# Kernel optimization log

Measured on AMD Instinct MI355X. Metric: run time of the kernel, lower is better.

## Reference

```python
import jax, jax.numpy as jnp
import numpy as np

N = 100000      # nodes
E = 1600000     # edges (avg degree 16)
D = 64          # in_dim == hidden_dim
L = 4           # layer_gin
G = 128         # graphs in batch
BN_EPS = 1e-5


def setup_inputs() -> dict:
    key = jax.random.key(0)
    ks = jax.random.split(key, 9)
    x = jax.random.normal(ks[0], (N, D), dtype=jnp.float32)
    edge_index = jax.random.randint(ks[1], (2, E), 0, N, dtype=jnp.int32)
    batch = jnp.sort(jax.random.randint(ks[2], (N,), 0, G, dtype=jnp.int32))
    s = 0.05
    W1 = jax.random.normal(ks[3], (L, D, D), dtype=jnp.float32) * s
    b1 = jax.random.normal(ks[4], (L, D), dtype=jnp.float32) * s
    gamma = jnp.ones((L, D), dtype=jnp.float32)
    beta = jnp.zeros((L, D), dtype=jnp.float32)
    W2 = jax.random.normal(ks[5], (L, D, D), dtype=jnp.float32) * s
    b2 = jax.random.normal(ks[6], (L, D), dtype=jnp.float32) * s
    return dict(x=x, edge_index=edge_index, batch=batch,
                W1=W1, b1=b1, gamma=gamma, beta=beta, W2=W2, b2=b2)


def reference(x, edge_index, batch, W1, b1, gamma, beta, W2, b2):
    n = x.shape[0]
    src, dst = edge_index[0], edge_index[1]  # flow source_to_target
    # in-degree for mean aggregation (clamped to avoid div-by-zero)
    deg = jax.ops.segment_sum(jnp.ones(src.shape, x.dtype), dst, num_segments=n)
    inv_deg = 1.0 / jnp.maximum(deg, 1.0)
    # graph sizes for global mean pool
    gcnt = jax.ops.segment_sum(jnp.ones((n,), x.dtype), batch, num_segments=G)
    inv_gcnt = 1.0 / jnp.maximum(gcnt, 1.0)

    h = x
    node_pool = jnp.zeros((n, W2.shape[-1]), x.dtype)
    g_pool = jnp.zeros((G, W2.shape[-1]), x.dtype)
    for l in range(L):  # small fixed layer count
        # scatter-mean neighbor aggregation: [E,D] gather -> segment_sum
        agg = jax.ops.segment_sum(h[src], dst, num_segments=n) * inv_deg[:, None]
        z = (h + agg) @ W1[l] + b1[l]          # eps=0: (1+eps)*x + mean_j x_j
        mu = z.mean(axis=0)
        var = z.var(axis=0)                     # biased, as torch BatchNorm1d
        z = (z - mu) * jax.lax.rsqrt(var + BN_EPS) * gamma[l] + beta[l]
        h = jax.nn.relu(z) @ W2[l] + b2[l]
        node_pool = node_pool + h
        g_pool = g_pool + jax.ops.segment_sum(h, batch, num_segments=G) * inv_gcnt[:, None]
    return node_pool, g_pool
```

## Files before the change

kernel.cpp:

```cpp
#include <hip/hip_runtime.h>

#define N_NODES 100000
#define N_EDGES 1600000
#define DIM 64
#define NLAYER 4
#define NGRAPH 128
#define BN_EPS 1e-5f
#define NSHARD 16

typedef unsigned short ushort_t;
typedef unsigned int uint_t;

__device__ __forceinline__ ushort_t f2bf(float f) {
    uint_t u = __float_as_uint(f);
    uint_t r = (u + 0x7FFFu + ((u >> 16) & 1u)) >> 16;
    return (ushort_t)r;
}

__device__ __forceinline__ void bf8_to_f32(const uint4 v, float f[8]) {
    f[0] = __uint_as_float(v.x << 16);
    f[1] = __uint_as_float(v.x & 0xFFFF0000u);
    f[2] = __uint_as_float(v.y << 16);
    f[3] = __uint_as_float(v.y & 0xFFFF0000u);
    f[4] = __uint_as_float(v.z << 16);
    f[5] = __uint_as_float(v.z & 0xFFFF0000u);
    f[6] = __uint_as_float(v.w << 16);
    f[7] = __uint_as_float(v.w & 0xFFFF0000u);
}


__global__ void k_hist(const int* __restrict__ ei, int* __restrict__ cntS,
                       int* __restrict__ rank) {
    int e = blockIdx.x * blockDim.x + threadIdx.x;
    if (e < N_EDGES) {
        int d = ei[N_EDGES + e];
        int s = blockIdx.x & (NSHARD - 1);
        rank[e] = atomicAdd(&cntS[s * N_NODES + d], 1);
    }
}

__global__ void k_sumsh(int* __restrict__ cntS, int* __restrict__ cnt) {
    int i = blockIdx.x * blockDim.x + threadIdx.x;
    if (i < N_NODES) {
        int run = 0;
#pragma unroll
        for (int s = 0; s < NSHARD; s++) {
            int c = cntS[s * N_NODES + i];
            cntS[s * N_NODES + i] = run;
            run += c;
        }
        cnt[i] = run;
    }
}

__global__ void k_scan1(const int* __restrict__ cnt, int* __restrict__ exc,
                        int* __restrict__ bsums) {
    __shared__ int s[256];
    int i = blockIdx.x * 256 + threadIdx.x;
    int v = (i < N_NODES) ? cnt[i] : 0;
    s[threadIdx.x] = v;
    __syncthreads();
    for (int off = 1; off < 256; off <<= 1) {
        int t = (threadIdx.x >= off) ? s[threadIdx.x - off] : 0;
        __syncthreads();
        s[threadIdx.x] += t;
        __syncthreads();
    }
    if (i < N_NODES) exc[i] = s[threadIdx.x] - v;
    if (threadIdx.x == 255) bsums[blockIdx.x] = s[255];
}

__global__ void k_scan2(const int* __restrict__ bsums, int* __restrict__ boffs, int nb) {
    __shared__ int s[512];
    int v = ((int)threadIdx.x < nb) ? bsums[threadIdx.x] : 0;
    s[threadIdx.x] = v;
    __syncthreads();
    for (int off = 1; off < 512; off <<= 1) {
        int t = (threadIdx.x >= off) ? s[threadIdx.x - off] : 0;
        __syncthreads();
        s[threadIdx.x] += t;
        __syncthreads();
    }
    if ((int)threadIdx.x < nb) boffs[threadIdx.x] = s[threadIdx.x] - v;
}

__global__ void k_scan3(int* __restrict__ exc, const int* __restrict__ boffs) {
    int i = blockIdx.x * 256 + threadIdx.x;
    if (i < N_NODES) exc[i] += boffs[blockIdx.x];
}

__global__ void k_fill(const int* __restrict__ ei, const int* __restrict__ rowptr,
                       const int* __restrict__ cntS, const int* __restrict__ rank,
                       int* __restrict__ csr) {
    int e = blockIdx.x * blockDim.x + threadIdx.x;
    if (e < N_EDGES) {
        int d = ei[N_EDGES + e];
        int s = blockIdx.x & (NSHARD - 1);
        csr[rowptr[d] + cntS[s * N_NODES + d] + rank[e]] = ei[e];
    }
}

__global__ void k_prep(const int* __restrict__ cnt, const int* __restrict__ batch,
                       float* __restrict__ invdeg, float* __restrict__ invg) {
    int i = blockIdx.x * blockDim.x + threadIdx.x;
    if (i < N_NODES) invdeg[i] = 1.0f / (float)max(cnt[i], 1);
    if (i < NGRAPH) {
        int key = i, lo = 0, hi = N_NODES;
        while (lo < hi) { int m = (lo + hi) >> 1; if (batch[m] < key) lo = m + 1; else hi = m; }
        int a = lo;
        key = i + 1; lo = 0; hi = N_NODES;
        while (lo < hi) { int m = (lo + hi) >> 1; if (batch[m] < key) lo = m + 1; else hi = m; }
        invg[i] = 1.0f / (float)max(lo - a, 1);
    }
}

__global__ void k_xcast(const float* __restrict__ x, ushort_t* __restrict__ xh) {
    int i = blockIdx.x * blockDim.x + threadIdx.x;
    if (i < N_NODES * 16) {
        const float4 v = ((const float4*)x)[i];
        ushort4 u;
        u.x = f2bf(v.x); u.y = f2bf(v.y); u.z = f2bf(v.z); u.w = f2bf(v.w);
        ((ushort4*)xh)[i] = u;
    }
}

__device__ __forceinline__ void grp8b(const ushort_t* __restrict__ h,
                                      const int* __restrict__ cp,
                                      int e, int deg, int q, int r,
                                      float acc[8]) {
    const int last = deg - 1;
    const int e0 = e + q;
    int i0 = cp[min(e0, last)];
    float m0 = (e0 < deg) ? 1.f : 0.f;
    const uint4 v = *(const uint4*)(h + (size_t)i0 * 64 + r * 8);
    float f[8];
    bf8_to_f32(v, f);
#pragma unroll
    for (int j = 0; j < 8; j++) acc[j] = fmaf(f[j], m0, acc[j]);
}


#define CHUNK_A 14

__global__ __launch_bounds__(256, 4)
void k_passA(const ushort_t* __restrict__ h, const float* __restrict__ W1,
             const float* __restrict__ b1,
             const int* __restrict__ rowptr, const int* __restrict__ cnt,
             const int* __restrict__ csr, const float* __restrict__ invdeg,
             float* __restrict__ z, float* __restrict__ colsum,
             float* __restrict__ colsumsq) {
    const int lane = threadIdx.x & 63;
    const int q = lane >> 3;
    const int r = lane & 7;
    int wid_raw = (blockIdx.x << 2) | (threadIdx.x >> 6);
    const int wid = __builtin_amdgcn_readfirstlane(wid_raw);
    const int n0 = wid * CHUNK_A;
    const int n1 = min(N_NODES, n0 + CHUNK_A);

    float w[64];
#pragma unroll
    for (int k = 0; k < 64; k++) w[k] = W1[k * 64 + lane];
#pragma unroll
    for (int k = 0; k < 64; k++) asm("" : "+v"(w[k]));
    const float bj = b1[lane];

    float ls = 0.f, lq = 0.f;
    for (int n = n0; n + 2 <= n1; n += 2) {
        const int sa = rowptr[n],     da = cnt[n];
        const int sb = rowptr[n + 1], db = cnt[n + 1];
        const float idga = invdeg[n], idgb = invdeg[n + 1];
        const int* __restrict__ ca = csr + sa;
        const int* __restrict__ cb = csr + sb;

        float aa[8] = {0,0,0,0,0,0,0,0};
        float ab[8] = {0,0,0,0,0,0,0,0};
        const int m = min(da, db);
        int e = 0;
        for (; e < m; e += 8) {
            grp8b(h, ca, e, da, q, r, aa);
            grp8b(h, cb, e, db, q, r, ab);
        }
        for (; e < da; e += 8) grp8b(h, ca, e, da, q, r, aa);
        for (; e < db; e += 8) grp8b(h, cb, e, db, q, r, ab);

#pragma unroll
        for (int j = 0; j < 8; j++) {
            aa[j] += __shfl_xor(aa[j], 8, 64);
            aa[j] += __shfl_xor(aa[j], 16, 64);
            aa[j] += __shfl_xor(aa[j], 32, 64);
            ab[j] += __shfl_xor(ab[j], 8, 64);
            ab[j] += __shfl_xor(ab[j], 16, 64);
            ab[j] += __shfl_xor(ab[j], 32, 64);
        }

        const uint4 sva = *(const uint4*)(h + (size_t)n * 64 + r * 8);
        const uint4 svb = *(const uint4*)(h + (size_t)(n + 1) * 64 + r * 8);
        float sa8[8], sb8[8];
        bf8_to_f32(sva, sa8);
        bf8_to_f32(svb, sb8);
        float ta[8], tb[8];
#pragma unroll
        for (int j = 0; j < 8; j++) {
            ta[j] = fmaf(aa[j], idga, sa8[j]);
            tb[j] = fmaf(ab[j], idgb, sb8[j]);
        }

        float za = bj, zb = bj;
#pragma unroll
        for (int rr = 0; rr < 8; rr++) {
#pragma unroll
            for (int j = 0; j < 8; j++) {
                float ka = __int_as_float(__builtin_amdgcn_readlane(__float_as_int(ta[j]), rr));
                float kb = __int_as_float(__builtin_amdgcn_readlane(__float_as_int(tb[j]), rr));
                za = fmaf(ka, w[rr * 8 + j], za);
                zb = fmaf(kb, w[rr * 8 + j], zb);
            }
        }
        z[(size_t)n * 64 + lane] = za;
        z[(size_t)(n + 1) * 64 + lane] = zb;
        ls += za + zb;
        lq += za * za + zb * zb;
    }

    __shared__ float rs[256], rq[256];
    rs[threadIdx.x] = ls;
    rq[threadIdx.x] = lq;
    __syncthreads();
    if (threadIdx.x < 64) {
        float a = rs[threadIdx.x] + rs[threadIdx.x + 64] + rs[threadIdx.x + 128] + rs[threadIdx.x + 192];
        float b = rq[threadIdx.x] + rq[threadIdx.x + 64] + rq[threadIdx.x + 128] + rq[threadIdx.x + 192];
        atomicAdd(&colsum[threadIdx.x], a);
        atomicAdd(&colsumsq[threadIdx.x], b);
    }
}


__global__ void k_bnprep(float* __restrict__ colsum, float* __restrict__ colsumsq,
                         const float* __restrict__ gamma, const float* __restrict__ beta,
                         float* __restrict__ scale, float* __restrict__ shift) {
    int j = threadIdx.x;
    float invn = 1.0f / (float)N_NODES;
    float mu = colsum[j] * invn;
    float var = colsumsq[j] * invn - mu * mu;
    float rsg = rsqrtf(var + BN_EPS);
    float sc = gamma[j] * rsg;
    scale[j] = sc;
    shift[j] = beta[j] - mu * sc;
    colsum[j] = 0.f;
    colsumsq[j] = 0.f;
}


#define CHUNK_M 28

__global__ __launch_bounds__(256, 4)
void k_passB(const float* __restrict__ z, const float* __restrict__ W2,
             const float* __restrict__ b2, const float* __restrict__ scale,
             const float* __restrict__ shift, const int* __restrict__ batch,
             ushort_t* __restrict__ hout, float* __restrict__ node_pool,
             float* __restrict__ gacc, int first) {
    const int lane = threadIdx.x & 63;
    int wid_raw = (blockIdx.x << 2) | (threadIdx.x >> 6);
    const int wid = __builtin_amdgcn_readfirstlane(wid_raw);
    const int n0 = wid * CHUNK_M;
    const int n1 = min(N_NODES, n0 + CHUNK_M);

    float w[64];
#pragma unroll
    for (int k = 0; k < 64; k++) w[k] = W2[k * 64 + lane];
#pragma unroll
    for (int k = 0; k < 64; k++) asm("" : "+v"(w[k]));
    const float bj = b2[lane], sc = scale[lane], sh = shift[lane];

    int curg = -1;
    float ga = 0.f;
    for (int n = n0; n + 4 <= n1; n += 4) {
        float ra = fmaxf(fmaf(z[(size_t)n * 64 + lane], sc, sh), 0.f);
        float rb = fmaxf(fmaf(z[(size_t)(n + 1) * 64 + lane], sc, sh), 0.f);
        float rc = fmaxf(fmaf(z[(size_t)(n + 2) * 64 + lane], sc, sh), 0.f);
        float rd = fmaxf(fmaf(z[(size_t)(n + 3) * 64 + lane], sc, sh), 0.f);
        float ha = bj, hb = bj, hc = bj, hd = bj;
#pragma unroll
        for (int k = 0; k < 64; k++) {
            float ka = __int_as_float(__builtin_amdgcn_readlane(__float_as_int(ra), k));
            float kb = __int_as_float(__builtin_amdgcn_readlane(__float_as_int(rb), k));
            float kc = __int_as_float(__builtin_amdgcn_readlane(__float_as_int(rc), k));
            float kd = __int_as_float(__builtin_amdgcn_readlane(__float_as_int(rd), k));
            ha = fmaf(ka, w[k], ha);
            hb = fmaf(kb, w[k], hb);
            hc = fmaf(kc, w[k], hc);
            hd = fmaf(kd, w[k], hd);
        }
        hout[(size_t)n * 64 + lane] = f2bf(ha);
        hout[(size_t)(n + 1) * 64 + lane] = f2bf(hb);
        hout[(size_t)(n + 2) * 64 + lane] = f2bf(hc);
        hout[(size_t)(n + 3) * 64 + lane] = f2bf(hd);
        if (first) {
            node_pool[(size_t)n * 64 + lane] = ha;
            node_pool[(size_t)(n + 1) * 64 + lane] = hb;
            node_pool[(size_t)(n + 2) * 64 + lane] = hc;
            node_pool[(size_t)(n + 3) * 64 + lane] = hd;
        } else {
            node_pool[(size_t)n * 64 + lane] += ha;
            node_pool[(size_t)(n + 1) * 64 + lane] += hb;
            node_pool[(size_t)(n + 2) * 64 + lane] += hc;
            node_pool[(size_t)(n + 3) * 64 + lane] += hd;
        }
        float hv[4] = {ha, hb, hc, hd};
#pragma unroll
        for (int j = 0; j < 4; j++) {
            int g = batch[n + j];
            if (g != curg) {
                if (curg >= 0) atomicAdd(&gacc[curg * 64 + lane], ga);
                ga = 0.f;
                curg = g;
            }
            ga += hv[j];
        }
    }
    if (curg >= 0) atomicAdd(&gacc[curg * 64 + lane], ga);
}

__global__ void k_gfinal(const float* __restrict__ gacc, const float* __restrict__ invg,
                         float* __restrict__ gout) {
    int i = blockIdx.x * blockDim.x + threadIdx.x;
    if (i < NGRAPH * 64) gout[i] = gacc[i] * invg[i >> 6];
}


extern "C" void kernel_launch(void* const* d_in, const int* in_sizes, int n_in,
                              void* d_out, int out_size, void* d_ws, size_t ws_size,
                              hipStream_t stream) {
    (void)in_sizes; (void)n_in; (void)out_size; (void)ws_size;
    const float* x     = (const float*)d_in[0];
    const int*   ei    = (const int*)d_in[1];
    const int*   batch = (const int*)d_in[2];
    const float* W1    = (const float*)d_in[3];
    const float* b1    = (const float*)d_in[4];
    const float* gamma = (const float*)d_in[5];
    const float* beta  = (const float*)d_in[6];
    const float* W2    = (const float*)d_in[7];
    const float* b2    = (const float*)d_in[8];
    float* out = (float*)d_out;

    size_t o = 0;
    size_t o_cntS    = o; o += (size_t)NSHARD * N_NODES;
    size_t o_colsum  = o; o += 64;
    size_t o_colsq   = o; o += 64;
    size_t o_gacc    = o; o += (size_t)NGRAPH * 64;
    size_t zero_elems = o;
    size_t o_cnt     = o; o += N_NODES;
    size_t o_rowptr  = o; o += N_NODES;
    size_t o_bsums   = o; o += 512;
    size_t o_boffs   = o; o += 512;
    size_t o_invdeg  = o; o += N_NODES;
    size_t o_invg    = o; o += NGRAPH;
    size_t o_scale   = o; o += 64;
    size_t o_shift   = o; o += 64;
    size_t o_rank    = o; o += N_EDGES;
    size_t o_csr     = o; o += N_EDGES;
    size_t o_bufA    = o; o += (size_t)N_NODES * 64;
    size_t o_bufB    = o; o += (size_t)N_NODES * 16;
    size_t o_xh      = o; o += (size_t)N_NODES * 16;

    int*   wsi = (int*)d_ws;
    float* wsf = (float*)d_ws;
    int*      cntS   = wsi + o_cntS;
    float*    colsum = wsf + o_colsum;
    float*    colsq  = wsf + o_colsq;
    float*    gacc   = wsf + o_gacc;
    int*      cnt    = wsi + o_cnt;
    int*      rowptr = wsi + o_rowptr;
    int*      bsums  = wsi + o_bsums;
    int*      boffs  = wsi + o_boffs;
    float*    invdeg = wsf + o_invdeg;
    float*    invg   = wsf + o_invg;
    float*    scale  = wsf + o_scale;
    float*    shift  = wsf + o_shift;
    int*      rank   = wsi + o_rank;
    int*      csr    = wsi + o_csr;
    float*    bufA   = wsf + o_bufA;
    ushort_t* bufB   = (ushort_t*)(wsi + o_bufB);
    ushort_t* xh     = (ushort_t*)(wsi + o_xh);

    hipMemsetAsync(d_ws, 0, zero_elems * 4, stream);

    const int eb = (N_EDGES + 255) / 256;
    const int nb = (N_NODES + 255) / 256;

    k_hist<<<eb, 256, 0, stream>>>(ei, cntS, rank);
    k_xcast<<<(N_NODES * 16 + 255) / 256, 256, 0, stream>>>(x, xh);
    k_sumsh<<<nb, 256, 0, stream>>>(cntS, cnt);
    k_scan1<<<nb, 256, 0, stream>>>(cnt, rowptr, bsums);
    k_scan2<<<1, 512, 0, stream>>>(bsums, boffs, nb);
    k_scan3<<<nb, 256, 0, stream>>>(rowptr, boffs);
    k_prep<<<nb, 256, 0, stream>>>(cnt, batch, invdeg, invg);
    k_fill<<<eb, 256, 0, stream>>>(ei, rowptr, cntS, rank, csr);

    const int gridA = (N_NODES + CHUNK_A * 4 - 1) / (CHUNK_A * 4);
    const int gridM = (N_NODES + CHUNK_M * 4 - 1) / (CHUNK_M * 4);
    for (int l = 0; l < NLAYER; l++) {
        const ushort_t* h_in = (l == 0) ? xh : bufB;
        k_passA<<<gridA, 256, 0, stream>>>(h_in, W1 + l * 4096, b1 + l * 64,
                                           rowptr, cnt, csr, invdeg,
                                           bufA, colsum, colsq);
        k_bnprep<<<1, 64, 0, stream>>>(colsum, colsq, gamma + l * 64, beta + l * 64,
                                       scale, shift);
        k_passB<<<gridM, 256, 0, stream>>>(bufA, W2 + l * 4096, b2 + l * 64,
                                           scale, shift, batch,
                                           bufB, out, gacc, (l == 0) ? 1 : 0);
    }
    k_gfinal<<<32, 256, 0, stream>>>(gacc, invg, out + (size_t)N_NODES * 64);
}
```

Before: 669.1 us.

## Split aggregation from MLP and switch to feature-major transposed layouts

The fused gather+GEMM kernel becomes three steps. A gather kernel writes the aggregated features in bf16, transposed to feature-major through shared memory. An MLP kernel assigns one node per lane with 64 accumulators and uniform weight loads, replacing the cross-lane readlane broadcasts. BN moments move to a separate column-reduction kernel over the transposed z. The aim is to drop the per-node readlane/VGPR-weight overhead, at the cost of extra launches, an extra pass over z, and bf16 rounding of the MLP input.

```diff
diff --git a/kernel.cpp b/kernel.cpp
--- a/kernel.cpp
+++ b/kernel.cpp
@@ -16,7 +16,9 @@
     uint_t r = (u + 0x7FFFu + ((u >> 16) & 1u)) >> 16;
     return (ushort_t)r;
 }
-
+__device__ __forceinline__ float bf2f(uint_t u) {
+    return __uint_as_float(u << 16);
+}
 __device__ __forceinline__ void bf8_to_f32(const uint4 v, float f[8]) {
     f[0] = __uint_as_float(v.x << 16);
     f[1] = __uint_as_float(v.x & 0xFFFF0000u);
@@ -140,32 +142,24 @@
 }
 
 
-#define CHUNK_A 14
+#define AGG_CHUNK 16
 
 __global__ __launch_bounds__(256, 4)
-void k_passA(const ushort_t* __restrict__ h, const float* __restrict__ W1,
-             const float* __restrict__ b1,
-             const int* __restrict__ rowptr, const int* __restrict__ cnt,
-             const int* __restrict__ csr, const float* __restrict__ invdeg,
-             float* __restrict__ z, float* __restrict__ colsum,
-             float* __restrict__ colsumsq) {
+void k_agg(const ushort_t* __restrict__ h, const int* __restrict__ rowptr,
+           const int* __restrict__ cnt, const int* __restrict__ csr,
+           const float* __restrict__ invdeg, ushort_t* __restrict__ tT) {
+    __shared__ ushort_t sm[4][AGG_CHUNK * 66];
+    const int w = threadIdx.x >> 6;
     const int lane = threadIdx.x & 63;
     const int q = lane >> 3;
     const int r = lane & 7;
-    int wid_raw = (blockIdx.x << 2) | (threadIdx.x >> 6);
-    const int wid = __builtin_amdgcn_readfirstlane(wid_raw);
-    const int n0 = wid * CHUNK_A;
-    const int n1 = min(N_NODES, n0 + CHUNK_A);
-
-    float w[64];
-#pragma unroll
-    for (int k = 0; k < 64; k++) w[k] = W1[k * 64 + lane];
-#pragma unroll
-    for (int k = 0; k < 64; k++) asm("" : "+v"(w[k]));
-    const float bj = b1[lane];
-
-    float ls = 0.f, lq = 0.f;
-    for (int n = n0; n + 2 <= n1; n += 2) {
+    const int wid = __builtin_amdgcn_readfirstlane((blockIdx.x << 2) | w);
+    if (wid >= N_NODES / AGG_CHUNK) return;
+    const int n0 = wid * AGG_CHUNK;
+    ushort_t* my = sm[w];
+
+    for (int pp = 0; pp < AGG_CHUNK; pp += 2) {
+        const int n = n0 + pp;
         const int sa = rowptr[n],     da = cnt[n];
         const int sb = rowptr[n + 1], db = cnt[n + 1];
         const float idga = invdeg[n], idgb = invdeg[n + 1];
@@ -205,32 +199,82 @@
             tb[j] = fmaf(ab[j], idgb, sb8[j]);
         }
 
-        float za = bj, zb = bj;
-#pragma unroll
-        for (int rr = 0; rr < 8; rr++) {
-#pragma unroll
-            for (int j = 0; j < 8; j++) {
-                float ka = __int_as_float(__builtin_amdgcn_readlane(__float_as_int(ta[j]), rr));
-                float kb = __int_as_float(__builtin_amdgcn_readlane(__float_as_int(tb[j]), rr));
-                za = fmaf(ka, w[rr * 8 + j], za);
-                zb = fmaf(kb, w[rr * 8 + j], zb);
+        if (q < 2) {
+            const int row = pp + q;
+            uint_t* dst = (uint_t*)&my[row * 66 + r * 8];
+#pragma unroll
+            for (int j2 = 0; j2 < 4; j2++) {
+                float lo = q ? tb[2 * j2] : ta[2 * j2];
+                float hi = q ? tb[2 * j2 + 1] : ta[2 * j2 + 1];
+                dst[j2] = (uint_t)f2bf(lo) | ((uint_t)f2bf(hi) << 16);
             }
         }
-        z[(size_t)n * 64 + lane] = za;
-        z[(size_t)(n + 1) * 64 + lane] = zb;
-        ls += za + zb;
-        lq += za * za + zb * zb;
-    }
-
+    }
+
+    const int nn = lane & 15;
+    const int hi = lane >> 4;
+    for (int kk = 0; kk < 64; kk += 4) {
+        const int k = kk + hi;
+        const uint_t v = *(const uint_t*)&my[nn * 66 + (k & ~1)];
+        const uint_t bits = (k & 1) ? (v >> 16) : (v & 0xFFFFu);
+        tT[(size_t)k * N_NODES + n0 + nn] = (ushort_t)bits;
+    }
+}
+
+
+__global__ __launch_bounds__(256, 4)
+void k_mlp1(const ushort_t* __restrict__ tT, const float* __restrict__ W1,
+            const float* __restrict__ b1, float* __restrict__ zT) {
+    const int lane = threadIdx.x & 63;
+    const int wid = __builtin_amdgcn_readfirstlane((blockIdx.x << 2) | (threadIdx.x >> 6));
+    const int n0 = wid * 64;
+    if (n0 >= N_NODES) return;
+    const int n = n0 + lane;
+    const int nc = min(n, N_NODES - 1);
+
+    float acc[64];
+#pragma unroll
+    for (int o = 0; o < 64; o++) acc[o] = 0.f;
+
+    for (int k = 0; k < 64; k++) {
+        const float tk = bf2f(tT[(size_t)k * N_NODES + nc]);
+        const float* __restrict__ Wr = W1 + (k << 6);
+#pragma unroll
+        for (int o = 0; o < 64; o++) acc[o] = fmaf(tk, Wr[o], acc[o]);
+    }
+    if (n < N_NODES) {
+#pragma unroll
+        for (int o = 0; o < 64; o++)
+            zT[(size_t)o * N_NODES + n] = acc[o] + b1[o];
+    }
+}
+
+
+__global__ void k_moments(const float* __restrict__ zT, float* __restrict__ colsum,
+                          float* __restrict__ colsumsq) {
+    const int row = blockIdx.x >> 3;
+    const int part = blockIdx.x & 7;
+    const float4* src = (const float4*)(zT + (size_t)row * N_NODES) + part * 3125;
+    float s = 0.f, sq = 0.f;
+    for (int i = threadIdx.x; i < 3125; i += 256) {
+        const float4 v = src[i];
+        s += (v.x + v.y) + (v.z + v.w);
+        sq += (v.x * v.x + v.y * v.y) + (v.z * v.z + v.w * v.w);
+    }
     __shared__ float rs[256], rq[256];
-    rs[threadIdx.x] = ls;
-    rq[threadIdx.x] = lq;
+    rs[threadIdx.x] = s;
+    rq[threadIdx.x] = sq;
     __syncthreads();
-    if (threadIdx.x < 64) {
-        float a = rs[threadIdx.x] + rs[threadIdx.x + 64] + rs[threadIdx.x + 128] + rs[threadIdx.x + 192];
-        float b = rq[threadIdx.x] + rq[threadIdx.x + 64] + rq[threadIdx.x + 128] + rq[threadIdx.x + 192];
-        atomicAdd(&colsum[threadIdx.x], a);
-        atomicAdd(&colsumsq[threadIdx.x], b);
+    for (int off = 128; off > 0; off >>= 1) {
+        if ((int)threadIdx.x < off) {
+            rs[threadIdx.x] += rs[threadIdx.x + off];
+            rq[threadIdx.x] += rq[threadIdx.x + off];
+        }
+        __syncthreads();
+    }
+    if (threadIdx.x == 0) {
+        atomicAdd(&colsum[row], rs[0]);
+        atomicAdd(&colsumsq[row], rq[0]);
     }
 }
 
@@ -251,72 +295,60 @@
 }
 
 
-#define CHUNK_M 28
-
 __global__ __launch_bounds__(256, 4)
-void k_passB(const float* __restrict__ z, const float* __restrict__ W2,
-             const float* __restrict__ b2, const float* __restrict__ scale,
-             const float* __restrict__ shift, const int* __restrict__ batch,
-             ushort_t* __restrict__ hout, float* __restrict__ node_pool,
-             float* __restrict__ gacc, int first) {
+void k_mlp2(const float* __restrict__ zT, const float* __restrict__ W2,
+            const float* __restrict__ b2, const float* __restrict__ scale,
+            const float* __restrict__ shift, const int* __restrict__ batch,
+            ushort_t* __restrict__ hout, float* __restrict__ node_pool,
+            float* __restrict__ gacc, int first) {
+    __shared__ ushort_t sm[4][64 * 66];
+    const int w = threadIdx.x >> 6;
     const int lane = threadIdx.x & 63;
-    int wid_raw = (blockIdx.x << 2) | (threadIdx.x >> 6);
-    const int wid = __builtin_amdgcn_readfirstlane(wid_raw);
-    const int n0 = wid * CHUNK_M;
-    const int n1 = min(N_NODES, n0 + CHUNK_M);
-
-    float w[64];
-#pragma unroll
-    for (int k = 0; k < 64; k++) w[k] = W2[k * 64 + lane];
-#pragma unroll
-    for (int k = 0; k < 64; k++) asm("" : "+v"(w[k]));
-    const float bj = b2[lane], sc = scale[lane], sh = shift[lane];
-
+    const int wid = __builtin_amdgcn_readfirstlane((blockIdx.x << 2) | (threadIdx.x >> 6));
+    const int n0 = wid * 64;
+    if (n0 >= N_NODES) return;
+    const int n = n0 + lane;
+    const int nc = min(n, N_NODES - 1);
+
+    float acc[64];
+#pragma unroll
+    for (int o = 0; o < 64; o++) acc[o] = 0.f;
+
+    for (int k = 0; k < 64; k++) {
+        const float zk = zT[(size_t)k * N_NODES + nc];
+        const float rv = fmaxf(fmaf(zk, scale[k], shift[k]), 0.f);
+        const float* __restrict__ Wr = W2 + (k << 6);
+#pragma unroll
+        for (int o = 0; o < 64; o++) acc[o] = fmaf(rv, Wr[o], acc[o]);
+    }
+
+    uint_t* dst = (uint_t*)&sm[w][lane * 66];
+#pragma unroll
+    for (int j2 = 0; j2 < 32; j2++) {
+        float lo = acc[2 * j2] + b2[2 * j2];
+        float hi = acc[2 * j2 + 1] + b2[2 * j2 + 1];
+        dst[j2] = (uint_t)f2bf(lo) | ((uint_t)f2bf(hi) << 16);
+    }
+
+    const int cntn = min(64, N_NODES - n0);
     int curg = -1;
     float ga = 0.f;
-    for (int n = n0; n + 4 <= n1; n += 4) {
-        float ra = fmaxf(fmaf(z[(size_t)n * 64 + lane], sc, sh), 0.f);
-        float rb = fmaxf(fmaf(z[(size_t)(n + 1) * 64 + lane], sc, sh), 0.f);
-        float rc = fmaxf(fmaf(z[(size_t)(n + 2) * 64 + lane], sc, sh), 0.f);
-        float rd = fmaxf(fmaf(z[(size_t)(n + 3) * 64 + lane], sc, sh), 0.f);
-        float ha = bj, hb = bj, hc = bj, hd = bj;
-#pragma unroll
-        for (int k = 0; k < 64; k++) {
-            float ka = __int_as_float(__builtin_amdgcn_readlane(__float_as_int(ra), k));
-            float kb = __int_as_float(__builtin_amdgcn_readlane(__float_as_int(rb), k));
-            float kc = __int_as_float(__builtin_amdgcn_readlane(__float_as_int(rc), k));
-            float kd = __int_as_float(__builtin_amdgcn_readlane(__float_as_int(rd), k));
-            ha = fmaf(ka, w[k], ha);
-            hb = fmaf(kb, w[k], hb);
-            hc = fmaf(kc, w[k], hc);
-            hd = fmaf(kd, w[k], hd);
-        }
-        hout[(size_t)n * 64 + lane] = f2bf(ha);
-        hout[(size_t)(n + 1) * 64 + lane] = f2bf(hb);
-        hout[(size_t)(n + 2) * 64 + lane] = f2bf(hc);
-        hout[(size_t)(n + 3) * 64 + lane] = f2bf(hd);
-        if (first) {
-            node_pool[(size_t)n * 64 + lane] = ha;
-            node_pool[(size_t)(n + 1) * 64 + lane] = hb;
-            node_pool[(size_t)(n + 2) * 64 + lane] = hc;
-            node_pool[(size_t)(n + 3) * 64 + lane] = hd;
-        } else {
-            node_pool[(size_t)n * 64 + lane] += ha;
-            node_pool[(size_t)(n + 1) * 64 + lane] += hb;
-            node_pool[(size_t)(n + 2) * 64 + lane] += hc;
-            node_pool[(size_t)(n + 3) * 64 + lane] += hd;
-        }
-        float hv[4] = {ha, hb, hc, hd};
-#pragma unroll
-        for (int j = 0; j < 4; j++) {
-            int g = batch[n + j];
-            if (g != curg) {
-                if (curg >= 0) atomicAdd(&gacc[curg * 64 + lane], ga);
-                ga = 0.f;
-                curg = g;
-            }
-            ga += hv[j];
-        }
+    for (int nn = 0; nn < cntn; nn++) {
+        const uint_t v = *(const uint_t*)&sm[w][nn * 66 + (lane & 62)];
+        const uint_t bits = (lane & 1) ? (v >> 16) : (v & 0xFFFFu);
+        const float hv = __uint_as_float(bits << 16);
+        const int node = n0 + nn;
+        const size_t off = (size_t)node * 64 + lane;
+        if (first) node_pool[off] = hv;
+        else node_pool[off] += hv;
+        hout[off] = (ushort_t)bits;
+        const int g = batch[node];
+        if (g != curg) {
+            if (curg >= 0) atomicAdd(&gacc[curg * 64 + lane], ga);
+            ga = 0.f;
+            curg = g;
+        }
+        ga += hv;
     }
     if (curg >= 0) atomicAdd(&gacc[curg * 64 + lane], ga);
 }
@@ -357,10 +389,11 @@
     size_t o_invg    = o; o += NGRAPH;
     size_t o_scale   = o; o += 64;
     size_t o_shift   = o; o += 64;
-    size_t o_rank    = o; o += N_EDGES;
     size_t o_csr     = o; o += N_EDGES;
-    size_t o_bufA    = o; o += (size_t)N_NODES * 64;
-    size_t o_bufB    = o; o += (size_t)N_NODES * 16;
+    size_t o_rank    = o;
+    size_t o_tT      = o; o += (size_t)64 * N_NODES / 2;
+    size_t o_zT      = o; o += (size_t)64 * N_NODES;
+    size_t o_hbuf    = o; o += (size_t)N_NODES * 16;
     size_t o_xh      = o; o += (size_t)N_NODES * 16;
 
     int*   wsi = (int*)d_ws;
@@ -377,10 +410,11 @@
     float*    invg   = wsf + o_invg;
     float*    scale  = wsf + o_scale;
     float*    shift  = wsf + o_shift;
+    int*      csr    = wsi + o_csr;
     int*      rank   = wsi + o_rank;
-    int*      csr    = wsi + o_csr;
-    float*    bufA   = wsf + o_bufA;
-    ushort_t* bufB   = (ushort_t*)(wsi + o_bufB);
+    ushort_t* tT     = (ushort_t*)(wsi + o_tT);
+    float*    zT     = wsf + o_zT;
+    ushort_t* hbuf   = (ushort_t*)(wsi + o_hbuf);
     ushort_t* xh     = (ushort_t*)(wsi + o_xh);
 
     hipMemsetAsync(d_ws, 0, zero_elems * 4, stream);
@@ -397,18 +431,18 @@
     k_prep<<<nb, 256, 0, stream>>>(cnt, batch, invdeg, invg);
     k_fill<<<eb, 256, 0, stream>>>(ei, rowptr, cntS, rank, csr);
 
-    const int gridA = (N_NODES + CHUNK_A * 4 - 1) / (CHUNK_A * 4);
-    const int gridM = (N_NODES + CHUNK_M * 4 - 1) / (CHUNK_M * 4);
+    const int aggBlocks = (N_NODES / AGG_CHUNK + 3) / 4;
+    const int mlpBlocks = ((N_NODES + 63) / 64 + 3) / 4;
     for (int l = 0; l < NLAYER; l++) {
-        const ushort_t* h_in = (l == 0) ? xh : bufB;
-        k_passA<<<gridA, 256, 0, stream>>>(h_in, W1 + l * 4096, b1 + l * 64,
-                                           rowptr, cnt, csr, invdeg,
-                                           bufA, colsum, colsq);
+        const ushort_t* h_in = (l == 0) ? xh : hbuf;
+        k_agg<<<aggBlocks, 256, 0, stream>>>(h_in, rowptr, cnt, csr, invdeg, tT);
+        k_mlp1<<<mlpBlocks, 256, 0, stream>>>(tT, W1 + l * 4096, b1 + l * 64, zT);
+        k_moments<<<512, 256, 0, stream>>>(zT, colsum, colsq);
         k_bnprep<<<1, 64, 0, stream>>>(colsum, colsq, gamma + l * 64, beta + l * 64,
                                        scale, shift);
-        k_passB<<<gridM, 256, 0, stream>>>(bufA, W2 + l * 4096, b2 + l * 64,
-                                           scale, shift, batch,
-                                           bufB, out, gacc, (l == 0) ? 1 : 0);
+        k_mlp2<<<mlpBlocks, 256, 0, stream>>>(zT, W2 + l * 4096, b2 + l * 64,
+                                              scale, shift, batch,
+                                              hbuf, out, gacc, (l == 0) ? 1 : 0);
     }
     k_gfinal<<<32, 256, 0, stream>>>(gacc, invg, out + (size_t)N_NODES * 64);
 }
```

Result: slower. 762.2 us (+13.9%).

## Replace readlane FMA matmul in aggregation pass with bf16 MFMA tiles

Applied to the files above, without the earlier changes.

The first-layer GEMM in the aggregation kernel moves from per-lane FMA with readlane broadcasts to MFMA 16x16x32 bf16 instructions. Each wave now aggregates 16 nodes, stages the (h+agg) rows as bf16 in shared memory, and multiplies them against W1 fragments that every block converts to bf16 in LDS. The 64 W1 registers per lane are gone, which should ease register pressure. The cost is a per-block W1 conversion, an extra rounding of activations to bf16 before the matmul, and column statistics reduced through shared-memory atomics.

```diff
diff --git a/kernel.cpp b/kernel.cpp
--- a/kernel.cpp
+++ b/kernel.cpp
@@ -7,16 +7,18 @@
 #define NGRAPH 128
 #define BN_EPS 1e-5f
 #define NSHARD 16
+#define AGG_CHUNK 16
 
 typedef unsigned short ushort_t;
 typedef unsigned int uint_t;
+typedef __attribute__((ext_vector_type(8))) short short8;
+typedef __attribute__((ext_vector_type(4))) float f32x4;
 
 __device__ __forceinline__ ushort_t f2bf(float f) {
     uint_t u = __float_as_uint(f);
     uint_t r = (u + 0x7FFFu + ((u >> 16) & 1u)) >> 16;
     return (ushort_t)r;
 }
-
 __device__ __forceinline__ void bf8_to_f32(const uint4 v, float f[8]) {
     f[0] = __uint_as_float(v.x << 16);
     f[1] = __uint_as_float(v.x & 0xFFFF0000u);
@@ -140,8 +142,6 @@
 }
 
 
-#define CHUNK_A 14
-
 __global__ __launch_bounds__(256, 4)
 void k_passA(const ushort_t* __restrict__ h, const float* __restrict__ W1,
              const float* __restrict__ b1,
@@ -149,88 +149,136 @@
              const int* __restrict__ csr, const float* __restrict__ invdeg,
              float* __restrict__ z, float* __restrict__ colsum,
              float* __restrict__ colsumsq) {
+    __shared__ ushort_t wfrag[512 * 8];
+    __shared__ uint_t smt[4][16 * 36];
+    __shared__ float red[128];
+
+    const int w = threadIdx.x >> 6;
     const int lane = threadIdx.x & 63;
     const int q = lane >> 3;
     const int r = lane & 7;
-    int wid_raw = (blockIdx.x << 2) | (threadIdx.x >> 6);
-    const int wid = __builtin_amdgcn_readfirstlane(wid_raw);
-    const int n0 = wid * CHUNK_A;
-    const int n1 = min(N_NODES, n0 + CHUNK_A);
-
-    float w[64];
-#pragma unroll
-    for (int k = 0; k < 64; k++) w[k] = W1[k * 64 + lane];
-#pragma unroll
-    for (int k = 0; k < 64; k++) asm("" : "+v"(w[k]));
-    const float bj = b1[lane];
-
-    float ls = 0.f, lq = 0.f;
-    for (int n = n0; n + 2 <= n1; n += 2) {
-        const int sa = rowptr[n],     da = cnt[n];
-        const int sb = rowptr[n + 1], db = cnt[n + 1];
-        const float idga = invdeg[n], idgb = invdeg[n + 1];
-        const int* __restrict__ ca = csr + sa;
-        const int* __restrict__ cb = csr + sb;
-
-        float aa[8] = {0,0,0,0,0,0,0,0};
-        float ab[8] = {0,0,0,0,0,0,0,0};
-        const int m = min(da, db);
-        int e = 0;
-        for (; e < m; e += 8) {
-            grp8b(h, ca, e, da, q, r, aa);
-            grp8b(h, cb, e, db, q, r, ab);
-        }
-        for (; e < da; e += 8) grp8b(h, ca, e, da, q, r, aa);
-        for (; e < db; e += 8) grp8b(h, cb, e, db, q, r, ab);
-
-#pragma unroll
-        for (int j = 0; j < 8; j++) {
-            aa[j] += __shfl_xor(aa[j], 8, 64);
-            aa[j] += __shfl_xor(aa[j], 16, 64);
-            aa[j] += __shfl_xor(aa[j], 32, 64);
-            ab[j] += __shfl_xor(ab[j], 8, 64);
-            ab[j] += __shfl_xor(ab[j], 16, 64);
-            ab[j] += __shfl_xor(ab[j], 32, 64);
-        }
-
-        const uint4 sva = *(const uint4*)(h + (size_t)n * 64 + r * 8);
-        const uint4 svb = *(const uint4*)(h + (size_t)(n + 1) * 64 + r * 8);
-        float sa8[8], sb8[8];
-        bf8_to_f32(sva, sa8);
-        bf8_to_f32(svb, sb8);
-        float ta[8], tb[8];
-#pragma unroll
-        for (int j = 0; j < 8; j++) {
-            ta[j] = fmaf(aa[j], idga, sa8[j]);
-            tb[j] = fmaf(ab[j], idgb, sb8[j]);
-        }
-
-        float za = bj, zb = bj;
-#pragma unroll
-        for (int rr = 0; rr < 8; rr++) {
+    const int wid = __builtin_amdgcn_readfirstlane((blockIdx.x << 2) | w);
+    const bool active = wid < (N_NODES / AGG_CHUNK);
+    const int n0 = (active ? wid : 0) * AGG_CHUNK;
+
+    for (int s = threadIdx.x; s < 512; s += 256) {
+        const int hh = s >> 8, c = (s >> 6) & 3, L = s & 63;
+        const int kb = hh * 32 + ((L >> 4) * 8);
+        const int out = c * 16 + (L & 15);
+        uint_t* dst = (uint_t*)&wfrag[s * 8];
+#pragma unroll
+        for (int j2 = 0; j2 < 4; j2++) {
+            const float lo = W1[(kb + 2 * j2) * 64 + out];
+            const float hi = W1[(kb + 2 * j2 + 1) * 64 + out];
+            dst[j2] = (uint_t)f2bf(lo) | ((uint_t)f2bf(hi) << 16);
+        }
+    }
+    if (threadIdx.x < 128) red[threadIdx.x] = 0.f;
+    __syncthreads();
+
+    if (active) {
+        for (int pp = 0; pp < AGG_CHUNK; pp += 2) {
+            const int n = n0 + pp;
+            const int sa = rowptr[n],     da = cnt[n];
+            const int sb = rowptr[n + 1], db = cnt[n + 1];
+            const float idga = invdeg[n], idgb = invdeg[n + 1];
+            const int* __restrict__ ca = csr + sa;
+            const int* __restrict__ cb = csr + sb;
+
+            float aa[8] = {0,0,0,0,0,0,0,0};
+            float ab[8] = {0,0,0,0,0,0,0,0};
+            const int mm = min(da, db);
+            int e = 0;
+            for (; e < mm; e += 8) {
+                grp8b(h, ca, e, da, q, r, aa);
+                grp8b(h, cb, e, db, q, r, ab);
+            }
+            for (; e < da; e += 8) grp8b(h, ca, e, da, q, r, aa);
+            for (; e < db; e += 8) grp8b(h, cb, e, db, q, r, ab);
+
 #pragma unroll
             for (int j = 0; j < 8; j++) {
-                float ka = __int_as_float(__builtin_amdgcn_readlane(__float_as_int(ta[j]), rr));
-                float kb = __int_as_float(__builtin_amdgcn_readlane(__float_as_int(tb[j]), rr));
-                za = fmaf(ka, w[rr * 8 + j], za);
-                zb = fmaf(kb, w[rr * 8 + j], zb);
-            }
-        }
-        z[(size_t)n * 64 + lane] = za;
-        z[(size_t)(n + 1) * 64 + lane] = zb;
-        ls += za + zb;
-        lq += za * za + zb * zb;
-    }
-
-    __shared__ float rs[256], rq[256];
-    rs[threadIdx.x] = ls;
-    rq[threadIdx.x] = lq;
+                aa[j] += __shfl_xor(aa[j], 8, 64);
+                aa[j] += __shfl_xor(aa[j], 16, 64);
+                aa[j] += __shfl_xor(aa[j], 32, 64);
+                ab[j] += __shfl_xor(ab[j], 8, 64);
+                ab[j] += __shfl_xor(ab[j], 16, 64);
+                ab[j] += __shfl_xor(ab[j], 32, 64);
+            }
+
+            const uint4 sva = *(const uint4*)(h + (size_t)n * 64 + r * 8);
+            const uint4 svb = *(const uint4*)(h + (size_t)(n + 1) * 64 + r * 8);
+            float sa8[8], sb8[8];
+            bf8_to_f32(sva, sa8);
+            bf8_to_f32(svb, sb8);
+            float ta[8], tb[8];
+#pragma unroll
+            for (int j = 0; j < 8; j++) {
+                ta[j] = fmaf(aa[j], idga, sa8[j]);
+                tb[j] = fmaf(ab[j], idgb, sb8[j]);
+            }
+
+            if (q < 2) {
+                const int row = pp + q;
+                uint_t* dst = &smt[w][row * 36 + r * 4];
+#pragma unroll
+                for (int j2 = 0; j2 < 4; j2++) {
+                    const float lo = q ? tb[2 * j2]     : ta[2 * j2];
+                    const float hi = q ? tb[2 * j2 + 1] : ta[2 * j2 + 1];
+                    dst[j2] = (uint_t)f2bf(lo) | ((uint_t)f2bf(hi) << 16);
+                }
+            }
+        }
+    }
+    __syncthreads();
+
+    const int m = lane & 15;
+    const int quad = lane >> 4;
+    const short8 a0 = *(const short8*)&smt[w][m * 36 + quad * 4];
+    const short8 a1 = *(const short8*)&smt[w][m * 36 + 16 + quad * 4];
+
+    float lsum[4], lsq[4];
+#pragma unroll
+    for (int c = 0; c < 4; c++) {
+        const short8 b0 = *(const short8*)&wfrag[(size_t)(c * 64 + lane) * 8];
+        const short8 b1f = *(const short8*)&wfrag[(size_t)((4 + c) * 64 + lane) * 8];
+        f32x4 D = {0.f, 0.f, 0.f, 0.f};
+        D = __builtin_amdgcn_mfma_f32_16x16x32_bf16(a0, b0, D, 0, 0, 0);
+        D = __builtin_amdgcn_mfma_f32_16x16x32_bf16(a1, b1f, D, 0, 0, 0);
+        const float bv = b1[c * 16 + m];
+        float s = 0.f, sq = 0.f;
+#pragma unroll
+        for (int reg = 0; reg < 4; reg++) {
+            const float zv = D[reg] + bv;
+            if (active) {
+                const int node = n0 + quad * 4 + reg;
+                z[(size_t)node * 64 + c * 16 + m] = zv;
+            }
+            s += zv;
+            sq += zv * zv;
+        }
+        lsum[c] = s;
+        lsq[c] = sq;
+    }
+
+    if (active) {
+#pragma unroll
+        for (int c = 0; c < 4; c++) {
+            float s = lsum[c], sq = lsq[c];
+            s += __shfl_xor(s, 16, 64);
+            s += __shfl_xor(s, 32, 64);
+            sq += __shfl_xor(sq, 16, 64);
+            sq += __shfl_xor(sq, 32, 64);
+            if (quad == 0) {
+                atomicAdd(&red[c * 16 + m], s);
+                atomicAdd(&red[64 + c * 16 + m], sq);
+            }
+        }
+    }
     __syncthreads();
     if (threadIdx.x < 64) {
-        float a = rs[threadIdx.x] + rs[threadIdx.x + 64] + rs[threadIdx.x + 128] + rs[threadIdx.x + 192];
-        float b = rq[threadIdx.x] + rq[threadIdx.x + 64] + rq[threadIdx.x + 128] + rq[threadIdx.x + 192];
-        atomicAdd(&colsum[threadIdx.x], a);
-        atomicAdd(&colsumsq[threadIdx.x], b);
+        atomicAdd(&colsum[threadIdx.x], red[threadIdx.x]);
+        atomicAdd(&colsumsq[threadIdx.x], red[64 + threadIdx.x]);
     }
 }
 
@@ -397,7 +445,7 @@
     k_prep<<<nb, 256, 0, stream>>>(cnt, batch, invdeg, invg);
     k_fill<<<eb, 256, 0, stream>>>(ei, rowptr, cntS, rank, csr);
 
-    const int gridA = (N_NODES + CHUNK_A * 4 - 1) / (CHUNK_A * 4);
+    const int gridA = (N_NODES / AGG_CHUNK + 3) / 4;
     const int gridM = (N_NODES + CHUNK_M * 4 - 1) / (CHUNK_M * 4);
     for (int l = 0; l < NLAYER; l++) {
         const ushort_t* h_in = (l == 0) ? xh : bufB;
```

Measured after the change: 648.5 us. 1.03x faster.
